# Optimization experiments

Hardware: AMD Instinct MI355X
Metric: run time of the kernel (lower is better)

Reference implementation:

```python
import jax, jax.numpy as jnp
import numpy as np

N_NODES = 20000
N_EDGES = 320000
EMB = 128


def setup_inputs() -> dict:
    key = jax.random.key(0)
    ks = jax.random.split(key, 8)
    h = jax.random.normal(ks[0], (N_NODES, EMB), dtype=jnp.float32)
    W1 = jax.random.normal(ks[1], (2 * EMB, 4 * EMB), dtype=jnp.float32) / np.sqrt(2 * EMB)
    b1 = jnp.zeros((4 * EMB,), dtype=jnp.float32)
    W2 = jax.random.normal(ks[2], (4 * EMB, 1), dtype=jnp.float32) / np.sqrt(4 * EMB)
    b2 = jnp.zeros((1,), dtype=jnp.float32)
    # logistic-noise uniforms for RelaxedBernoulli rsample, kept away from {0,1}
    u = jax.random.uniform(ks[3], (N_EDGES,), dtype=jnp.float32, minval=1e-6, maxval=1.0 - 1e-6)
    row = jax.random.randint(ks[4], (N_EDGES,), 0, N_NODES, dtype=jnp.int32)
    col = jax.random.randint(ks[5], (N_EDGES,), 0, N_NODES, dtype=jnp.int32)
    edge_mask = -jnp.ones((N_EDGES,), dtype=jnp.int32)  # torch code initializes mask to -1
    return {"h": h, "W1": W1, "b1": b1, "W2": W2, "b2": b2,
            "u": u, "row": row, "col": col, "edge_mask": edge_mask, "hierarchy": 0}


def _segment_softmax(scores, seg, num_segments):
    m = jax.ops.segment_max(scores, seg, num_segments=num_segments)
    e = jnp.exp(scores - m[seg])
    s = jax.ops.segment_sum(e, seg, num_segments=num_segments)
    return e / s[seg]


TEMPERATURE = 1.0
RATIO = 0.5  # threshold for hard bernoulli


def reference(h, W1, b1, W2, b2, u, row, col, edge_mask, hierarchy):
    # edge gather + concat: [E, 2*EMB]
    edge_rep = jnp.concatenate([h[row], h[col]], axis=-1)
    # 2-layer MLP edge scorer -> [E]
    hid = jax.nn.relu(edge_rep @ W1 + b1)
    scores = (hid @ W2 + b2).reshape(-1)
    # segment softmax over edges grouped by source node (torch: softmax(edge_score, edge_index[0]))
    probs = _segment_softmax(scores, row, N_NODES)
    # RelaxedBernoulli(temperature, probs).rsample(): sigmoid((logits + logistic)/T)
    logits = jnp.log(probs) - jnp.log1p(-probs)
    logistic = jnp.log(u) - jnp.log1p(-u)
    y = jax.nn.sigmoid((logits + logistic) / TEMPERATURE)
    y_hard = (y > RATIO).astype(y.dtype)
    y_st = jax.lax.stop_gradient(y_hard - y) + y  # straight-through
    # edge_mask[y == 1] = hierarchy + 1
    new_mask = jnp.where(y_st == 1.0, jnp.int32(hierarchy + 1), edge_mask)
    c_idx = new_mask > 0
    s_idx = new_mask == -1
    causal_w = jnp.where(c_idx, scores, 0.0)
    spu_w = jnp.where(s_idx, -scores, 0.0)
    return scores, y_st, new_mask, causal_w, spu_w
```

## Files before the change

kernel.cpp:

```cpp
#include <hip/hip_runtime.h>
#include <math.h>

#define N_NODES 20000
#define N_EDGES 320000
#define EMB 128
#define HID 512
#define ROWS_PER_BLOCK 16
#define SC_CAP 2048
#define NCHUNK ((N_NODES + 1023) / 1024)

typedef float v2f __attribute__((ext_vector_type(2)));

#if defined(__has_builtin)
#if __has_builtin(__builtin_elementwise_fma)
#define V2FMA(a, b, c) __builtin_elementwise_fma((a), (b), (c))
#else
#define V2FMA(a, b, c) ((a) * (b) + (c))
#endif
#else
#define V2FMA(a, b, c) ((a) * (b) + (c))
#endif

__global__ void init_deg(int* __restrict__ deg, int* __restrict__ offs) {
    int i = blockIdx.x * 256 + threadIdx.x;
    if (i < N_NODES) deg[i] = 0;
    if (i == 0) offs[N_NODES] = N_EDGES;
}

#define TM 128
#define TN 128
#define BK 8
#define NTILES (EMB / BK)
#define GEMM_MT ((N_NODES + TM - 1) / TM)
#define GEMM_BLOCKS (8 * GEMM_MT)
#define HIST_BLOCKS ((N_EDGES + 255) / 256)

__global__ __launch_bounds__(256) void gemm_hist(
    const float* __restrict__ h, const float* __restrict__ W1,
    const float* __restrict__ b1, float* __restrict__ P, float* __restrict__ Q,
    const int* __restrict__ row, int* __restrict__ deg)
{
    const int bid = blockIdx.x;
    const int tid = threadIdx.x;

    if (bid >= GEMM_BLOCKS) {
        const int e = (bid - GEMM_BLOCKS) * 256 + tid;
        if (e < N_EDGES) atomicAdd(&deg[row[e]], 1);
        return;
    }

    __shared__ float As[2][BK][TM + 4];
    __shared__ float Bs[2][BK][TN];

    const int nt = bid & 7;
    const int mt = bid >> 3;
    const int m_base = mt * TM;

    const int a_m = tid >> 1;
    const int a_k = (tid & 1) << 2;
    const int  row_a = m_base + a_m;
    const bool a_ok  = row_a < N_NODES;
    const float* __restrict__ hrow = h + (size_t)row_a * EMB + a_k;

    const int b_k = tid >> 5;
    const int b_n = (tid & 31) << 2;
    const int w_row_off = (nt < 4) ? 0 : 128;
    const int w_col     = (nt & 3) * TN + b_n;
    const float* __restrict__ wrow = W1 + (size_t)(w_row_off + b_k) * HID + w_col;

    const int ty = tid >> 4, tx = tid & 15;
    const int cm = ty << 2, cn = tx << 2;

    v2f acc[8][4] = {};

    float4 pa, pb;
    pa = make_float4(0.f, 0.f, 0.f, 0.f);
    if (a_ok) pa = *(const float4*)(hrow);
    pb = *(const float4*)(wrow);
    As[0][a_k + 0][a_m] = pa.x;
    As[0][a_k + 1][a_m] = pa.y;
    As[0][a_k + 2][a_m] = pa.z;
    As[0][a_k + 3][a_m] = pa.w;
    *(float4*)&Bs[0][b_k][b_n] = pb;
    __syncthreads();

    for (int t = 0; t < NTILES; ++t) {
        const int cur = t & 1;
        if (t + 1 < NTILES) {
            const int k0 = (t + 1) * BK;
            pa = make_float4(0.f, 0.f, 0.f, 0.f);
            if (a_ok) pa = *(const float4*)(hrow + k0);
            pb = *(const float4*)(wrow + (size_t)k0 * HID);
        }

#pragma unroll
        for (int kk = 0; kk < BK; ++kk) {
            float a[8];
            *(float4*)&a[0] = *(const float4*)&As[cur][kk][cm];
            *(float4*)&a[4] = *(const float4*)&As[cur][kk][cm + 64];
            float4 b0 = *(const float4*)&Bs[cur][kk][cn];
            float4 b1v = *(const float4*)&Bs[cur][kk][cn + 64];
            v2f bp[4] = {(v2f){b0.x, b0.y}, (v2f){b0.z, b0.w},
                         (v2f){b1v.x, b1v.y}, (v2f){b1v.z, b1v.w}};
#pragma unroll
            for (int i = 0; i < 8; ++i) {
                v2f ai = (v2f){a[i], a[i]};
#pragma unroll
                for (int j = 0; j < 4; ++j)
                    acc[i][j] = V2FMA(ai, bp[j], acc[i][j]);
            }
        }

        if (t + 1 < NTILES) {
            const int nxt = 1 - cur;
            As[nxt][a_k + 0][a_m] = pa.x;
            As[nxt][a_k + 1][a_m] = pa.y;
            As[nxt][a_k + 2][a_m] = pa.z;
            As[nxt][a_k + 3][a_m] = pa.w;
            *(float4*)&Bs[nxt][b_k][b_n] = pb;
            __syncthreads();
        }
    }

    const bool  isP = (nt < 4);
    const int   col_base = (nt & 3) * TN;
    float* __restrict__ dstbase = isP ? P : Q;

    v2f bias[4] = {{0.f,0.f},{0.f,0.f},{0.f,0.f},{0.f,0.f}};
    if (isP) {
        float4 bv0 = *(const float4*)(b1 + col_base + cn);
        float4 bv1 = *(const float4*)(b1 + col_base + cn + 64);
        bias[0] = (v2f){bv0.x, bv0.y};
        bias[1] = (v2f){bv0.z, bv0.w};
        bias[2] = (v2f){bv1.x, bv1.y};
        bias[3] = (v2f){bv1.z, bv1.w};
    }

#pragma unroll
    for (int i = 0; i < 8; ++i) {
        const int r = m_base + cm + (i < 4 ? i : 64 + i - 4);
        if (r < N_NODES) {
            float* dst = dstbase + (size_t)r * HID + col_base;
            v2f c0 = acc[i][0] + bias[0], c1 = acc[i][1] + bias[1];
            v2f c2 = acc[i][2] + bias[2], c3 = acc[i][3] + bias[3];
            *(float4*)(dst + cn)      = make_float4(c0.x, c0.y, c1.x, c1.y);
            *(float4*)(dst + cn + 64) = make_float4(c2.x, c2.y, c3.x, c3.y);
        }
    }
}

__device__ __forceinline__ int wave_incl_scan(int v, int lane) {
#pragma unroll
    for (int off = 1; off < 64; off <<= 1) {
        int t = __shfl_up(v, off, 64);
        if (lane >= off) v += t;
    }
    return v;
}

__global__ __launch_bounds__(1024) void scan_part(const int* __restrict__ deg,
                                                  int* __restrict__ part,
                                                  int* __restrict__ totals) {
    __shared__ int wsum[16];
    const int tid = threadIdx.x, lane = tid & 63, w = tid >> 6;
    const int i = blockIdx.x * 1024 + tid;
    int v = (i < N_NODES) ? deg[i] : 0;
    int incl = wave_incl_scan(v, lane);
    if (lane == 63) wsum[w] = incl;
    __syncthreads();
    if (w == 0) {
        int x = (lane < 16) ? wsum[lane] : 0;
        int xs = wave_incl_scan(x, lane);
        if (lane < 16) wsum[lane] = xs - x;
        if (lane == 15) totals[blockIdx.x] = xs;
    }
    __syncthreads();
    if (i < N_NODES) part[i] = wsum[w] + incl - v;
}

__global__ __launch_bounds__(1024) void scan_apply(const int* __restrict__ part,
                                                   const int* __restrict__ totals,
                                                   int* __restrict__ cursor,
                                                   int* __restrict__ offs) {
    __shared__ int carry_s;
    const int tid = threadIdx.x;
    if (tid < 64) {
        int v = (tid < NCHUNK) ? totals[tid] : 0;
        int incl = wave_incl_scan(v, tid);
        if (tid == (int)blockIdx.x) carry_s = incl - v;
    }
    __syncthreads();
    const int i = blockIdx.x * 1024 + tid;
    if (i < N_NODES) {
        int o = part[i] + carry_s;
        cursor[i] = o;
        offs[i] = o;
    }
}

__global__ void scatter_edges(const int* __restrict__ row, const int* __restrict__ col,
                              int* __restrict__ cursor,
                              unsigned short* __restrict__ cols16,
                              int* __restrict__ inv) {
    int e = blockIdx.x * 256 + threadIdx.x;
    if (e >= N_EDGES) return;
    int r = row[e];
    int pos = atomicAdd(&cursor[r], 1);
    cols16[pos] = (unsigned short)col[e];
    inv[e] = pos;
}

__global__ __launch_bounds__(256) void fused_edge(
    const float* __restrict__ P, const float* __restrict__ Q,
    const float* __restrict__ W2, const float* __restrict__ b2,
    const unsigned short* __restrict__ cols16, const int* __restrict__ offs,
    float2* __restrict__ tmp)
{
    __shared__ float sc_lds[SC_CAP];

    const int r0 = blockIdx.x * ROWS_PER_BLOCK;
    const int r1 = (r0 + ROWS_PER_BLOCK < N_NODES) ? r0 + ROWS_PER_BLOCK : N_NODES;
    const int e0 = offs[r0];
    const int tid = threadIdx.x, lane = tid & 63, w = tid >> 6;
    const int j0 = lane << 2;

    const float4 w0 = *(const float4*)(W2 + j0);
    const float4 w1 = *(const float4*)(W2 + 256 + j0);
    const float bias2 = b2[0];

    for (int r = r0 + w; r < r1; r += 4) {
        const int es = offs[r], ee = offs[r + 1];
        const int d = ee - es;
        if (d == 0) continue;

        const float* __restrict__ prow = P + (size_t)r * HID;
        const float4 p0 = *(const float4*)(prow + j0);
        const float4 p1 = *(const float4*)(prow + 256 + j0);

        for (int base = 0; base < d; base += 64) {
            const int nch = (d - base < 64) ? d - base : 64;
            int mycol = 0;
            if (lane < nch) mycol = (int)cols16[es + base + lane];

#define QL(k, bb, d0, d1) { \
                int c_ = __shfl(mycol, (bb) + (k), 64); \
                const float* __restrict__ q_ = Q + (size_t)c_ * HID; \
                d0 = *(const float4*)(q_ + j0); \
                d1 = *(const float4*)(q_ + 256 + j0); }

            float4 q00,q01,q10,q11,q20,q21,q30,q31;
            QL(0,0,q00,q01); QL(1,0,q10,q11); QL(2,0,q20,q21); QL(3,0,q30,q31);

            for (int b = 0; b < nch; b += 4) {
                float4 n00,n01,n10,n11,n20,n21,n30,n31;
                const bool more = (b + 4) < nch;
                if (more) {
                    QL(0,b+4,n00,n01); QL(1,b+4,n10,n11);
                    QL(2,b+4,n20,n21); QL(3,b+4,n30,n31);
                }

                float s0, s1, s2, s3;
#define DOT8(qa, qb, sd) { \
                    float t_ = 0.0f; \
                    t_ = fmaf(fmaxf(p0.x + qa.x, 0.0f), w0.x, t_); \
                    t_ = fmaf(fmaxf(p0.y + qa.y, 0.0f), w0.y, t_); \
                    t_ = fmaf(fmaxf(p0.z + qa.z, 0.0f), w0.z, t_); \
                    t_ = fmaf(fmaxf(p0.w + qa.w, 0.0f), w0.w, t_); \
                    t_ = fmaf(fmaxf(p1.x + qb.x, 0.0f), w1.x, t_); \
                    t_ = fmaf(fmaxf(p1.y + qb.y, 0.0f), w1.y, t_); \
                    t_ = fmaf(fmaxf(p1.z + qb.z, 0.0f), w1.z, t_); \
                    t_ = fmaf(fmaxf(p1.w + qb.w, 0.0f), w1.w, t_); \
                    sd = t_; }
                DOT8(q00,q01,s0); DOT8(q10,q11,s1);
                DOT8(q20,q21,s2); DOT8(q30,q31,s3);

#pragma unroll
                for (int off = 32; off > 0; off >>= 1) {
                    s0 += __shfl_down(s0, off, 64);
                    s1 += __shfl_down(s1, off, 64);
                    s2 += __shfl_down(s2, off, 64);
                    s3 += __shfl_down(s3, off, 64);
                }

                if (lane == 0) {
                    const int nv = nch - b;
                    const int libase = es - e0 + base + b;
                    { float sc = s0 + bias2; int li = libase;
                      if (li < SC_CAP) sc_lds[li] = sc; else tmp[e0 + li].x = sc; }
                    if (nv > 1) { float sc = s1 + bias2; int li = libase + 1;
                      if (li < SC_CAP) sc_lds[li] = sc; else tmp[e0 + li].x = sc; }
                    if (nv > 2) { float sc = s2 + bias2; int li = libase + 2;
                      if (li < SC_CAP) sc_lds[li] = sc; else tmp[e0 + li].x = sc; }
                    if (nv > 3) { float sc = s3 + bias2; int li = libase + 3;
                      if (li < SC_CAP) sc_lds[li] = sc; else tmp[e0 + li].x = sc; }
                }

                if (more) {
                    q00=n00; q01=n01; q10=n10; q11=n11;
                    q20=n20; q21=n21; q30=n30; q31=n31;
                }
            }
#undef QL
#undef DOT8
        }

        float m = -INFINITY;
        for (int j = lane; j < d; j += 64) {
            const int li = es - e0 + j;
            float s = (li < SC_CAP) ? sc_lds[li] : tmp[es + j].x;
            m = fmaxf(m, s);
        }
#pragma unroll
        for (int off = 32; off > 0; off >>= 1)
            m = fmaxf(m, __shfl_down(m, off, 64));
        m = __shfl(m, 0, 64);

        float ssum = 0.0f;
        for (int j = lane; j < d; j += 64) {
            const int li = es - e0 + j;
            float s = (li < SC_CAP) ? sc_lds[li] : tmp[es + j].x;
            ssum += expf(s - m);
        }
#pragma unroll
        for (int off = 32; off > 0; off >>= 1)
            ssum += __shfl_down(ssum, off, 64);
        ssum = __shfl(ssum, 0, 64);

        for (int j = lane; j < d; j += 64) {
            const int li = es - e0 + j;
            float s = (li < SC_CAP) ? sc_lds[li] : tmp[es + j].x;
            float p = expf(s - m) / ssum;
            float logits = logf(p) - log1pf(-p);
            tmp[es + j] = make_float2(s, logits);
        }
    }
}

__global__ __launch_bounds__(256) void unperm(
    const float2* __restrict__ tmp, const int* __restrict__ inv,
    const float* __restrict__ u, const int* __restrict__ edge_mask,
    const int* __restrict__ hierarchy,
    float* __restrict__ scores, float* __restrict__ out_y,
    float* __restrict__ out_mask, float* __restrict__ out_causal,
    float* __restrict__ out_spu)
{
    const int e = blockIdx.x * 256 + threadIdx.x;
    if (e >= N_EDGES) return;
    const float2 t = tmp[inv[e]];
    const float s = t.x;
    const float uu = u[e];
    const float L = logf(uu) - log1pf(-uu);
    const float y = 1.0f / (1.0f + expf(-(t.y + L)));
    const bool hard = y > 0.5f;
    const int mm = hard ? (hierarchy[0] + 1) : edge_mask[e];
    scores[e]     = s;
    out_y[e]      = hard ? 1.0f : 0.0f;
    out_mask[e]   = (float)mm;
    out_causal[e] = (mm > 0)   ?  s : 0.0f;
    out_spu[e]    = (mm == -1) ? -s : 0.0f;
}

extern "C" void kernel_launch(void* const* d_in, const int* in_sizes, int n_in,
                              void* d_out, int out_size, void* d_ws, size_t ws_size,
                              hipStream_t stream) {
    const float* h_ptr = (const float*)d_in[0];
    const float* W1    = (const float*)d_in[1];
    const float* b1    = (const float*)d_in[2];
    const float* W2    = (const float*)d_in[3];
    const float* b2    = (const float*)d_in[4];
    const float* u     = (const float*)d_in[5];
    const int*   row   = (const int*)d_in[6];
    const int*   col   = (const int*)d_in[7];
    const int*   emask = (const int*)d_in[8];
    const int*   hier  = (const int*)d_in[9];

    float* out        = (float*)d_out;
    float* scores     = out;
    float* out_y      = out + (size_t)N_EDGES;
    float* out_mask   = out + 2 * (size_t)N_EDGES;
    float* out_causal = out + 3 * (size_t)N_EDGES;
    float* out_spu    = out + 4 * (size_t)N_EDGES;

    float*          P      = (float*)d_ws;
    float*          Qm     = P + (size_t)N_NODES * HID;
    float2*         tmp    = (float2*)(Qm + (size_t)N_NODES * HID);
    unsigned short* cols16 = (unsigned short*)(tmp + N_EDGES);
    int*            inv    = (int*)(cols16 + N_EDGES);
    int*            deg    = inv + N_EDGES;
    int*            cursor = deg + N_NODES;
    int*            offs   = cursor + N_NODES;
    int*            part   = offs + N_NODES + 1;
    int*            totals = part + N_NODES;

    hipLaunchKernelGGL(init_deg, dim3((N_NODES + 255) / 256), dim3(256), 0, stream,
                       deg, offs);

    hipLaunchKernelGGL(gemm_hist, dim3(GEMM_BLOCKS + HIST_BLOCKS), dim3(256), 0, stream,
                       h_ptr, W1, b1, P, Qm, row, deg);

    hipLaunchKernelGGL(scan_part, dim3(NCHUNK), dim3(1024), 0, stream, deg, part, totals);
    hipLaunchKernelGGL(scan_apply, dim3(NCHUNK), dim3(1024), 0, stream,
                       part, totals, cursor, offs);
    hipLaunchKernelGGL(scatter_edges, dim3((N_EDGES + 255) / 256), dim3(256), 0, stream,
                       row, col, cursor, cols16, inv);

    hipLaunchKernelGGL(fused_edge, dim3((N_NODES + ROWS_PER_BLOCK - 1) / ROWS_PER_BLOCK),
                       dim3(256), 0, stream,
                       P, Qm, W2, b2, cols16, offs, tmp);

    hipLaunchKernelGGL(unperm, dim3((N_EDGES + 255) / 256), dim3(256), 0, stream,
                       tmp, inv, u, emask, hier,
                       scores, out_y, out_mask, out_causal, out_spu);
}
```

Baseline: 280.0 us.

## Keep per-row edge scores in registers and shrink fused_edge blocks

Reworks fused_edge so each wavefront owns a contiguous run of 4 rows in 128-thread blocks, with no shared-memory score buffer. For rows of degree up to 64, each lane keeps its edge's score in a register and the segment softmax is done with xor-shuffle reductions, avoiding LDS round trips and the serial lane-0 writes. Higher-degree rows fall back to staging scores in global tmp. The per-chunk prefetch depth drops from 4 to 2 edges, which lowers register pressure but exposes less memory-level parallelism per wave.

Measured after the change: 275.6 us. About the same (-1.6%).

```diff
diff --git a/kernel.cpp b/kernel.cpp
--- a/kernel.cpp
+++ b/kernel.cpp
@@ -5,9 +5,12 @@
 #define N_EDGES 320000
 #define EMB 128
 #define HID 512
-#define ROWS_PER_BLOCK 16
-#define SC_CAP 2048
 #define NCHUNK ((N_NODES + 1023) / 1024)
+
+#define RPW 4
+#define WPB 2
+#define RPB (RPW * WPB)
+#define FE_BLOCKS ((N_NODES + RPB - 1) / RPB)
 
 typedef float v2f __attribute__((ext_vector_type(2)));
 
@@ -210,25 +213,79 @@
     inv[e] = pos;
 }
 
-__global__ __launch_bounds__(256) void fused_edge(
+__device__ __forceinline__ float dot8_relu(const float4 qa, const float4 qb,
+                                           const float4 p0, const float4 p1,
+                                           const float4 w0, const float4 w1) {
+    float t = 0.0f;
+    t = fmaf(fmaxf(p0.x + qa.x, 0.0f), w0.x, t);
+    t = fmaf(fmaxf(p0.y + qa.y, 0.0f), w0.y, t);
+    t = fmaf(fmaxf(p0.z + qa.z, 0.0f), w0.z, t);
+    t = fmaf(fmaxf(p0.w + qa.w, 0.0f), w0.w, t);
+    t = fmaf(fmaxf(p1.x + qb.x, 0.0f), w1.x, t);
+    t = fmaf(fmaxf(p1.y + qb.y, 0.0f), w1.y, t);
+    t = fmaf(fmaxf(p1.z + qb.z, 0.0f), w1.z, t);
+    t = fmaf(fmaxf(p1.w + qb.w, 0.0f), w1.w, t);
+    return t;
+}
+
+__device__ __forceinline__ float chunk_scores(
+    const float* __restrict__ Q, const unsigned short* __restrict__ cols16,
+    int es_base, int nch, int lane, int j0,
+    const float4 p0, const float4 p1, const float4 w0, const float4 w1,
+    float bias2)
+{
+    int mycol = 0;
+    if (lane < nch) mycol = (int)cols16[es_base + lane];
+    float mysc = -INFINITY;
+
+#define QL2(k, bb, d0, d1) { \
+        int c_ = __shfl(mycol, (bb) + (k), 64); \
+        const float* __restrict__ q_ = Q + (size_t)c_ * HID; \
+        d0 = *(const float4*)(q_ + j0); \
+        d1 = *(const float4*)(q_ + 256 + j0); }
+
+    float4 a00, a01, a10, a11;
+    QL2(0, 0, a00, a01); QL2(1, 0, a10, a11);
+
+    for (int b = 0; b < nch; b += 2) {
+        float4 n00, n01, n10, n11;
+        const bool more = (b + 2) < nch;
+        if (more) { QL2(0, b + 2, n00, n01); QL2(1, b + 2, n10, n11); }
+
+        float s0 = dot8_relu(a00, a01, p0, p1, w0, w1);
+        float s1 = dot8_relu(a10, a11, p0, p1, w0, w1);
+
+#pragma unroll
+        for (int off = 32; off > 0; off >>= 1) {
+            s0 += __shfl_xor(s0, off, 64);
+            s1 += __shfl_xor(s1, off, 64);
+        }
+
+        const int k = lane - b;
+        if ((unsigned)k < 2u && lane < nch) mysc = (k ? s1 : s0) + bias2;
+
+        if (more) { a00 = n00; a01 = n01; a10 = n10; a11 = n11; }
+    }
+#undef QL2
+    return mysc;
+}
+
+__global__ __launch_bounds__(128) void fused_edge(
     const float* __restrict__ P, const float* __restrict__ Q,
     const float* __restrict__ W2, const float* __restrict__ b2,
     const unsigned short* __restrict__ cols16, const int* __restrict__ offs,
     float2* __restrict__ tmp)
 {
-    __shared__ float sc_lds[SC_CAP];
-
-    const int r0 = blockIdx.x * ROWS_PER_BLOCK;
-    const int r1 = (r0 + ROWS_PER_BLOCK < N_NODES) ? r0 + ROWS_PER_BLOCK : N_NODES;
-    const int e0 = offs[r0];
     const int tid = threadIdx.x, lane = tid & 63, w = tid >> 6;
+    const int r0 = blockIdx.x * RPB + w * RPW;
+    const int r1 = (r0 + RPW < N_NODES) ? r0 + RPW : N_NODES;
     const int j0 = lane << 2;
 
     const float4 w0 = *(const float4*)(W2 + j0);
     const float4 w1 = *(const float4*)(W2 + 256 + j0);
     const float bias2 = b2[0];
 
-    for (int r = r0 + w; r < r1; r += 4) {
+    for (int r = r0; r < r1; ++r) {
         const int es = offs[r], ee = offs[r + 1];
         const int d = ee - es;
         if (d == 0) continue;
@@ -237,101 +294,54 @@
         const float4 p0 = *(const float4*)(prow + j0);
         const float4 p1 = *(const float4*)(prow + 256 + j0);
 
-        for (int base = 0; base < d; base += 64) {
-            const int nch = (d - base < 64) ? d - base : 64;
-            int mycol = 0;
-            if (lane < nch) mycol = (int)cols16[es + base + lane];
-
-#define QL(k, bb, d0, d1) { \
-                int c_ = __shfl(mycol, (bb) + (k), 64); \
-                const float* __restrict__ q_ = Q + (size_t)c_ * HID; \
-                d0 = *(const float4*)(q_ + j0); \
-                d1 = *(const float4*)(q_ + 256 + j0); }
-
-            float4 q00,q01,q10,q11,q20,q21,q30,q31;
-            QL(0,0,q00,q01); QL(1,0,q10,q11); QL(2,0,q20,q21); QL(3,0,q30,q31);
-
-            for (int b = 0; b < nch; b += 4) {
-                float4 n00,n01,n10,n11,n20,n21,n30,n31;
-                const bool more = (b + 4) < nch;
-                if (more) {
-                    QL(0,b+4,n00,n01); QL(1,b+4,n10,n11);
-                    QL(2,b+4,n20,n21); QL(3,b+4,n30,n31);
-                }
-
-                float s0, s1, s2, s3;
-#define DOT8(qa, qb, sd) { \
-                    float t_ = 0.0f; \
-                    t_ = fmaf(fmaxf(p0.x + qa.x, 0.0f), w0.x, t_); \
-                    t_ = fmaf(fmaxf(p0.y + qa.y, 0.0f), w0.y, t_); \
-                    t_ = fmaf(fmaxf(p0.z + qa.z, 0.0f), w0.z, t_); \
-                    t_ = fmaf(fmaxf(p0.w + qa.w, 0.0f), w0.w, t_); \
-                    t_ = fmaf(fmaxf(p1.x + qb.x, 0.0f), w1.x, t_); \
-                    t_ = fmaf(fmaxf(p1.y + qb.y, 0.0f), w1.y, t_); \
-                    t_ = fmaf(fmaxf(p1.z + qb.z, 0.0f), w1.z, t_); \
-                    t_ = fmaf(fmaxf(p1.w + qb.w, 0.0f), w1.w, t_); \
-                    sd = t_; }
-                DOT8(q00,q01,s0); DOT8(q10,q11,s1);
-                DOT8(q20,q21,s2); DOT8(q30,q31,s3);
-
-#pragma unroll
-                for (int off = 32; off > 0; off >>= 1) {
-                    s0 += __shfl_down(s0, off, 64);
-                    s1 += __shfl_down(s1, off, 64);
-                    s2 += __shfl_down(s2, off, 64);
-                    s3 += __shfl_down(s3, off, 64);
-                }
-
-                if (lane == 0) {
-                    const int nv = nch - b;
-                    const int libase = es - e0 + base + b;
-                    { float sc = s0 + bias2; int li = libase;
-                      if (li < SC_CAP) sc_lds[li] = sc; else tmp[e0 + li].x = sc; }
-                    if (nv > 1) { float sc = s1 + bias2; int li = libase + 1;
-                      if (li < SC_CAP) sc_lds[li] = sc; else tmp[e0 + li].x = sc; }
-                    if (nv > 2) { float sc = s2 + bias2; int li = libase + 2;
-                      if (li < SC_CAP) sc_lds[li] = sc; else tmp[e0 + li].x = sc; }
-                    if (nv > 3) { float sc = s3 + bias2; int li = libase + 3;
-                      if (li < SC_CAP) sc_lds[li] = sc; else tmp[e0 + li].x = sc; }
-                }
-
-                if (more) {
-                    q00=n00; q01=n01; q10=n10; q11=n11;
-                    q20=n20; q21=n21; q30=n30; q31=n31;
-                }
+        if (d <= 64) {
+            float mysc = chunk_scores(Q, cols16, es, d, lane, j0,
+                                      p0, p1, w0, w1, bias2);
+
+            float m = mysc;
+#pragma unroll
+            for (int off = 32; off > 0; off >>= 1)
+                m = fmaxf(m, __shfl_xor(m, off, 64));
+
+            float ev = (lane < d) ? expf(mysc - m) : 0.0f;
+            float ssum = ev;
+#pragma unroll
+            for (int off = 32; off > 0; off >>= 1)
+                ssum += __shfl_xor(ssum, off, 64);
+
+            if (lane < d) {
+                float p = ev / ssum;
+                float logits = logf(p) - log1pf(-p);
+                tmp[es + lane] = make_float2(mysc, logits);
             }
-#undef QL
-#undef DOT8
-        }
-
-        float m = -INFINITY;
-        for (int j = lane; j < d; j += 64) {
-            const int li = es - e0 + j;
-            float s = (li < SC_CAP) ? sc_lds[li] : tmp[es + j].x;
-            m = fmaxf(m, s);
-        }
-#pragma unroll
-        for (int off = 32; off > 0; off >>= 1)
-            m = fmaxf(m, __shfl_down(m, off, 64));
-        m = __shfl(m, 0, 64);
-
-        float ssum = 0.0f;
-        for (int j = lane; j < d; j += 64) {
-            const int li = es - e0 + j;
-            float s = (li < SC_CAP) ? sc_lds[li] : tmp[es + j].x;
-            ssum += expf(s - m);
-        }
-#pragma unroll
-        for (int off = 32; off > 0; off >>= 1)
-            ssum += __shfl_down(ssum, off, 64);
-        ssum = __shfl(ssum, 0, 64);
-
-        for (int j = lane; j < d; j += 64) {
-            const int li = es - e0 + j;
-            float s = (li < SC_CAP) ? sc_lds[li] : tmp[es + j].x;
-            float p = expf(s - m) / ssum;
-            float logits = logf(p) - log1pf(-p);
-            tmp[es + j] = make_float2(s, logits);
+        } else {
+            for (int base = 0; base < d; base += 64) {
+                const int nch = (d - base < 64) ? d - base : 64;
+                float mysc = chunk_scores(Q, cols16, es + base, nch, lane, j0,
+                                          p0, p1, w0, w1, bias2);
+                if (lane < nch) tmp[es + base + lane].x = mysc;
+            }
+
+            float m = -INFINITY;
+            for (int j = lane; j < d; j += 64)
+                m = fmaxf(m, tmp[es + j].x);
+#pragma unroll
+            for (int off = 32; off > 0; off >>= 1)
+                m = fmaxf(m, __shfl_xor(m, off, 64));
+
+            float ssum = 0.0f;
+            for (int j = lane; j < d; j += 64)
+                ssum += expf(tmp[es + j].x - m);
+#pragma unroll
+            for (int off = 32; off > 0; off >>= 1)
+                ssum += __shfl_xor(ssum, off, 64);
+
+            for (int j = lane; j < d; j += 64) {
+                float s = tmp[es + j].x;
+                float p = expf(s - m) / ssum;
+                float logits = logf(p) - log1pf(-p);
+                tmp[es + j] = make_float2(s, logits);
+            }
         }
     }
 }
@@ -404,8 +414,7 @@
     hipLaunchKernelGGL(scatter_edges, dim3((N_EDGES + 255) / 256), dim3(256), 0, stream,
                        row, col, cursor, cols16, inv);
 
-    hipLaunchKernelGGL(fused_edge, dim3((N_NODES + ROWS_PER_BLOCK - 1) / ROWS_PER_BLOCK),
-                       dim3(256), 0, stream,
+    hipLaunchKernelGGL(fused_edge, dim3(FE_BLOCKS), dim3(128), 0, stream,
                        P, Qm, W2, b2, cols16, offs, tmp);
 
     hipLaunchKernelGGL(unperm, dim3((N_EDGES + 255) / 256), dim3(256), 0, stream,
```
